# Kernel tuning notes

Hardware: AMD Instinct MI355X
Metric: run time of the kernel (lower is better)

Reference implementation:

```python
import jax, jax.numpy as jnp
import numpy as np

N = 20000   # nodes
E = 320000  # edges
T = 12      # sequence_length
H = 64      # hidden_dim
CIN = 16    # input_dim_per_step
L = 3       # num_st_layers
BN_EPS = 1e-5


def setup_inputs() -> dict:
    key = jax.random.key(0)
    ks = jax.random.split(key, 30)
    s = 0.05
    rn = lambda k, shp: jax.random.normal(k, shp, jnp.float32) * s
    inp = {
        "x": jax.random.normal(ks[0], (N, T * CIN), jnp.float32),
        "edge_index": jax.random.randint(ks[1], (2, E), 0, N, jnp.int32),
        # embedding
        "We": rn(ks[2], (CIN, H)), "be": rn(ks[3], (H,)),
        # stacked per-layer params for the 3 ST layers
        "gcn_W": rn(ks[4], (L, H, H)), "gcn_b": rn(ks[5], (L, H)),
        "conv_w": rn(ks[6], (L, H, H, 3)), "conv_b": rn(ks[7], (L, H)),
        "bn_g": jnp.ones((L, H), jnp.float32), "bn_b": rn(ks[8], (L, H)),
        "bn_m": rn(ks[9], (L, H)),
        "bn_v": jax.random.uniform(ks[10], (L, H), jnp.float32, 0.5, 1.5),
        # temporal attention MLP (H -> H//2 -> 1)
        "ta_w1": rn(ks[11], (H, H // 2)), "ta_b1": rn(ks[12], (H // 2,)),
        "ta_w2": rn(ks[13], (H // 2, 1)), "ta_b2": rn(ks[14], (1,)),
        # feature attention MLP (T -> T//2 -> 1)
        "fa_w1": rn(ks[15], (T, T // 2)), "fa_b1": rn(ks[16], (T // 2,)),
        "fa_w2": rn(ks[17], (T // 2, 1)), "fa_b2": rn(ks[18], (1,)),
        # output MLP (H -> H//2 -> 1)
        "ow1": rn(ks[19], (H, H // 2)), "ob1": rn(ks[20], (H // 2,)),
        "ow2": rn(ks[21], (H // 2, 1)), "ob2": rn(ks[22], (1,)),
    }
    return inp


def reference(x, edge_index, We, be, gcn_W, gcn_b, conv_w, conv_b,
              bn_g, bn_b, bn_m, bn_v, ta_w1, ta_b1, ta_w2, ta_b2,
              fa_w1, fa_b1, fa_w2, fa_b2, ow1, ob1, ow2, ob2):
    n = x.shape[0]
    # --- GCN normalization with self-loops (PyG gcn_norm) ---
    loops = jnp.arange(n, dtype=edge_index.dtype)
    src = jnp.concatenate([edge_index[0], loops])
    dst = jnp.concatenate([edge_index[1], loops])
    deg = jax.ops.segment_sum(jnp.ones_like(src, jnp.float32), dst, num_segments=n)
    dinv = 1.0 / jnp.sqrt(deg)  # deg >= 1 thanks to self-loops
    coef = dinv[src] * dinv[dst]  # [E+N]

    # --- per-timestep embedding (vectorized over t) ---
    xr = x.reshape(n, T, CIN)
    emb = jax.nn.relu(jnp.einsum('ntc,ch->nth', xr, We) + be)  # [N,T,H]
    x_st = emb.reshape(n, T * H)

    # --- ST layers (replicating original row-major .view layout mixing) ---
    for i in range(L):
        xi = x_st.reshape(n, H, T)  # [N,C,T]
        # GCNConv per timestep, batched over t: linear then normalized aggregate
        h = jnp.einsum('nct,cd->ndt', xi, gcn_W[i])          # [N,H,T]
        msg = coef[:, None, None] * h[src]                   # [E+N,H,T]
        agg = jax.ops.segment_sum(msg, dst, num_segments=n) + gcn_b[i][None, :, None]
        # temporal conv (kernel 3, pad 1) over T
        tmp = jax.lax.conv_general_dilated(
            agg, conv_w[i], (1,), [(1, 1)],
            dimension_numbers=('NCH', 'OIH', 'NCH')) + conv_b[i][None, :, None]
        # BatchNorm1d (eval mode: running stats)
        normed = (tmp - bn_m[i][None, :, None]) / jnp.sqrt(bn_v[i][None, :, None] + BN_EPS)
        normed = normed * bn_g[i][None, :, None] + bn_b[i][None, :, None]
        # residual is Identity (in_channels == out_channels)
        x_st = jax.nn.relu(normed + xi).reshape(n, H * T)

    # --- dual attention pooling ---
    xa = x_st.reshape(n, T, H)
    tw = (jnp.einsum('ntm,mk->ntk', jax.nn.relu(jnp.einsum('nth,hm->ntm', xa, ta_w1) + ta_b1), ta_w2) + ta_b2)[..., 0]
    tw = jax.nn.softmax(tw, axis=1)                          # [N,T]
    xt = (xa * tw[..., None]).transpose(0, 2, 1)             # [N,H,T]
    fw = (jnp.einsum('nhm,mk->nhk', jax.nn.relu(jnp.einsum('nht,tm->nhm', xt, fa_w1) + fa_b1), fa_w2) + fa_b2)[..., 0]
    fw = jax.nn.softmax(fw, axis=1)                          # [N,H]
    x_final = jnp.sum(xt * fw[..., None], axis=2)            # [N,H]

    # --- output MLP (dropout is identity in eval) ---
    out = jax.nn.relu(x_final @ ow1 + ob1) @ ow2 + ob2       # [N,1]
    return out
```

## Files before the change

kernel.cpp:

```cpp
#include <hip/hip_runtime.h>
#include <cstddef>
#include <cstdint>

#define T_ 12
#define H_ 64
#define CIN_ 16
#define F_ 768
#define BN_EPS 1e-5f
#define ECAP 80
#define RPITCH 88
#define SLOTS 64

typedef float v2f __attribute__((ext_vector_type(2)));
typedef short s8v __attribute__((ext_vector_type(8)));
typedef float f4v __attribute__((ext_vector_type(4)));

__device__ __forceinline__ unsigned short f2bf(float f) {
    unsigned u = __float_as_uint(f);
    unsigned r = (u + 0x7FFFu + ((u >> 16) & 1u)) >> 16;
    return (unsigned short)r;
}
__device__ __forceinline__ float bf2f(unsigned short h) {
    return __uint_as_float(((unsigned)h) << 16);
}
__device__ __forceinline__ v2f bf2x2(unsigned u) {
    v2f r;
    r.x = __uint_as_float(u << 16);
    r.y = __uint_as_float(u & 0xFFFF0000u);
    return r;
}
__device__ __forceinline__ v2f pkfma(v2f a, v2f b, v2f c) {
    return __builtin_elementwise_fma(a, b, c);
}


__global__ void k_init(int* __restrict__ cursor, int n) {
    int i = blockIdx.x * 256 + threadIdx.x;
    if (i < n) cursor[i] = 0;
}


__global__ __launch_bounds__(256) void k_fused(
        const float* __restrict__ gcn_W, const float* __restrict__ gcn_b,
        const float* __restrict__ conv_w,
        float* __restrict__ wkp, float* __restrict__ bkp,
        const int* __restrict__ srcv, const int* __restrict__ dstv,
        int* __restrict__ cursor, int* __restrict__ csr_src, int e,
        const float* __restrict__ x, const float* __restrict__ We,
        const float* __restrict__ be, unsigned short* __restrict__ xbf, int nT,
        int nbE) {
    __shared__ float sW[CIN_ * H_];
    __shared__ float sb[H_];
    int b = blockIdx.x;
    int tid = threadIdx.x;

    if (b < 36) {
        int l = b / 12, k = (b / 4) % 3, cq = b & 3;
        const float* Wg = gcn_W + (size_t)l * 4096;
        const float* cw = conv_w + (size_t)l * 12288;
#pragma unroll
        for (int j = 0; j < 4; j++) {
            int idx = j * 256 + tid;
            int c = cq * 16 + (idx >> 6);
            int o = idx & 63;
            float acc = 0.f;
            for (int d = 0; d < 64; d++)
                acc += Wg[c * 64 + d] * cw[(size_t)(o * 64 + d) * 3 + k];
            wkp[(((size_t)l * 3 + k) * 64 + c) * 64 + o] = acc;
        }
        if (cq == 0 && tid < 64) {
            int o = tid;
            const float* gb = gcn_b + (size_t)l * 64;
            float acc = 0.f;
            for (int d = 0; d < 64; d++)
                acc += gb[d] * cw[(size_t)(o * 64 + d) * 3 + k];
            bkp[((size_t)l * 3 + k) * 64 + o] = acc;
        }
        return;
    }
    if (b < 36 + nbE) {
        int i = (b - 36) * 256 + tid;
        if (i < e) {
            int d = dstv[i], s = srcv[i];
            int pos = atomicAdd(&cursor[d], 1);
            if (pos < SLOTS) csr_src[d * SLOTS + pos] = s;
        }
        return;
    }
    for (int i = tid; i < CIN_ * H_; i += 256) sW[i] = We[i];
    if (tid < H_) sb[tid] = be[tid];
    __syncthreads();
    int h4  = tid & 15;
    int ntl = tid >> 4;
    int nt  = (b - 36 - nbE) * 16 + ntl;
    if (nt >= nT) return;
    const float4* xp = (const float4*)(x + (size_t)nt * CIN_);
    float4 xv4[4];
    xv4[0] = xp[0]; xv4[1] = xp[1]; xv4[2] = xp[2]; xv4[3] = xp[3];
    const float* xs = (const float*)xv4;
    float acc[4];
#pragma unroll
    for (int j = 0; j < 4; j++) acc[j] = sb[h4 * 4 + j];
#pragma unroll
    for (int c = 0; c < CIN_; c++) {
        float4 w = *(const float4*)&sW[c * H_ + h4 * 4];
        float xc = xs[c];
        acc[0] += xc * w.x; acc[1] += xc * w.y;
        acc[2] += xc * w.z; acc[3] += xc * w.w;
    }
    ushort4 h;
    h.x = f2bf(fmaxf(acc[0], 0.f)); h.y = f2bf(fmaxf(acc[1], 0.f));
    h.z = f2bf(fmaxf(acc[2], 0.f)); h.w = f2bf(fmaxf(acc[3], 0.f));
    *(ushort4*)&xbf[(size_t)nt * H_ + h4 * 4] = h;
}


__global__ __launch_bounds__(256) void k_post(
        const float* __restrict__ wkp, unsigned short* __restrict__ wkA,
        const int* __restrict__ cursor, const int* __restrict__ csr_src,
        float* __restrict__ csr_coef, float* __restrict__ dinv, int n) {
    int b = blockIdx.x;
    int tid = threadIdx.x;
    if (b < 18) {
        int wave = tid >> 6, lane = tid & 63;
        int job = b * 4 + wave;
        int l = job / 24, rem = job % 24;
        int mt = rem / 6, ks = rem % 6;
        int o = mt * 16 + (lane & 15);
        int kbase = ks * 32 + (lane >> 4) * 8;
#pragma unroll
        for (int j = 0; j < 8; j++) {
            int k = kbase + j;
            int kk = k >> 6, c = k & 63;
            float v = wkp[(((size_t)l * 3 + kk) * 64 + c) * 64 + o];
            wkA[((((size_t)l * 24) + mt * 6 + ks) * 64 + lane) * 8 + j] = f2bf(v);
        }
        return;
    }
    int i = (b - 18) * 256 + tid;
    int node = i >> 6, slot = i & 63;
    if (node >= n) return;
    int deg = cursor[node];
    float dn = rsqrtf((float)(deg + 1));
    if (slot == 0) dinv[node] = dn;
    if (slot < min(deg, SLOTS)) {
        int s = csr_src[node * SLOTS + slot];
        csr_coef[node * SLOTS + slot] = rsqrtf((float)(cursor[s] + 1)) * dn;
    }
}


#define EDGE_LOAD(P, Q0, Q1) { \
    const unsigned short* rp_ = xin + (size_t)(P).x * F_; \
    Q0 = *(const uint4*)(rp_ + (lane << 3)); \
    Q1 = *(const uint2*)(rp_ + 512 + (lane << 2)); }

#define EDGE_FMA(P, Q0, Q1) { \
    float c_ = __int_as_float((P).y); \
    v2f c2_ = {c_, c_}; \
    a0 = pkfma(bf2x2((Q0).x), c2_, a0); a1 = pkfma(bf2x2((Q0).y), c2_, a1); \
    a2 = pkfma(bf2x2((Q0).z), c2_, a2); a3 = pkfma(bf2x2((Q0).w), c2_, a3); \
    a4 = pkfma(bf2x2((Q1).x), c2_, a4); a5 = pkfma(bf2x2((Q1).y), c2_, a5); }

#define LAYER_GATHER_CONV()                                                    \
    int tid = threadIdx.x;                                                     \
    int n0 = blockIdx.x * 8;                                                   \
    int wave = tid >> 6, lane = tid & 63;                                      \
    int wbase = wave * (ECAP * 2);                                             \
    for (int i = tid; i < 8 * 2 * RPITCH; i += 256) {                          \
        int s = i / (2 * RPITCH);                                              \
        int r = i - s * (2 * RPITCH);                                          \
        int row = (r < RPITCH) ? 0 : 13;                                       \
        int c = (r < RPITCH) ? r : r - RPITCH;                                 \
        sxb[s * 14 * RPITCH + row * RPITCH + c] = 0;                           \
    }                                                                          \
    int begs[2], cnts[2], stgs[2], epos[2];                                    \
    {                                                                          \
        int pos = 0;                                                           \
        for (int si = 0; si < 2; si++) {                                       \
            int nn = n0 + wave * 2 + si; if (nn >= n) nn = n - 1;              \
            int beg = nn * SLOTS;                                              \
            int cnt = min(degv[nn], SLOTS);                                    \
            int stg = min(cnt, ECAP - pos);                                    \
            for (int i = lane; i < stg; i += 64) {                             \
                se[wbase + (pos + i) * 2]     = csr_src[beg + i];              \
                se[wbase + (pos + i) * 2 + 1] = __float_as_int(csr_coef[beg + i]); \
            }                                                                  \
            begs[si] = beg; cnts[si] = cnt; stgs[si] = stg; epos[si] = pos;    \
            pos += stg;                                                        \
        }                                                                      \
    }                                                                          \
    {                                                                          \
        int wof[12];                                                           \
        _Pragma("unroll")                                                      \
        for (int u = 0; u < 12; u++) {                                         \
            int idx = (u < 8) ? ((lane << 3) + u) : (512 + (lane << 2) + u - 8); \
            int c = idx / 12, t = idx - 12 * c;                                \
            wof[u] = (t + 1) * RPITCH + c;                                     \
        }                                                                      \
        for (int si = 0; si < 2; si++) {                                       \
            int s = wave * 2 + si;                                             \
            int nn = n0 + s; if (nn >= n) nn = n - 1;                          \
            float dn = dinv[nn];                                               \
            float cs = dn * dn;                                                \
            v2f cs2 = {cs, cs};                                                \
            const unsigned short* xr = xin + (size_t)nn * F_;                  \
            uint4 z0 = *(const uint4*)(xr + (lane << 3));                      \
            uint2 z1 = *(const uint2*)(xr + 512 + (lane << 2));                \
            v2f a0 = bf2x2(z0.x) * cs2, a1 = bf2x2(z0.y) * cs2;                \
            v2f a2 = bf2x2(z0.z) * cs2, a3 = bf2x2(z0.w) * cs2;                \
            v2f a4 = bf2x2(z1.x) * cs2, a5 = bf2x2(z1.y) * cs2;                \
            int cnt = stgs[si];                                                \
            int base = wbase + epos[si] * 2;                                   \
            int e = 0;                                                         \
            for (; e + 3 < cnt; e += 4) {                                      \
                int2 pA = *(const int2*)&se[base + e * 2];                     \
                int2 pB = *(const int2*)&se[base + e * 2 + 2];                 \
                int2 pC = *(const int2*)&se[base + e * 2 + 4];                 \
                int2 pD = *(const int2*)&se[base + e * 2 + 6];                 \
                uint4 qA0; uint2 qA1; EDGE_LOAD(pA, qA0, qA1)                  \
                uint4 qB0; uint2 qB1; EDGE_LOAD(pB, qB0, qB1)                  \
                uint4 qC0; uint2 qC1; EDGE_LOAD(pC, qC0, qC1)                  \
                uint4 qD0; uint2 qD1; EDGE_LOAD(pD, qD0, qD1)                  \
                EDGE_FMA(pA, qA0, qA1)                                         \
                EDGE_FMA(pB, qB0, qB1)                                         \
                EDGE_FMA(pC, qC0, qC1)                                         \
                EDGE_FMA(pD, qD0, qD1)                                         \
            }                                                                  \
            for (; e < cnt; e++) {                                             \
                int2 pA = *(const int2*)&se[base + e * 2];                     \
                uint4 qA0; uint2 qA1; EDGE_LOAD(pA, qA0, qA1)                  \
                EDGE_FMA(pA, qA0, qA1)                                         \
            }                                                                  \
            for (int g = begs[si] + stgs[si]; g < begs[si] + cnts[si]; g++) {  \
                int2 pA; pA.x = csr_src[g];                                    \
                pA.y = __float_as_int(csr_coef[g]);                            \
                uint4 qA0; uint2 qA1; EDGE_LOAD(pA, qA0, qA1)                  \
                EDGE_FMA(pA, qA0, qA1)                                         \
            }                                                                  \
            unsigned short* wp0 = &sxb[s * 14 * RPITCH];                       \
            wp0[wof[0]]  = f2bf(a0.x); wp0[wof[1]]  = f2bf(a0.y);              \
            wp0[wof[2]]  = f2bf(a1.x); wp0[wof[3]]  = f2bf(a1.y);              \
            wp0[wof[4]]  = f2bf(a2.x); wp0[wof[5]]  = f2bf(a2.y);              \
            wp0[wof[6]]  = f2bf(a3.x); wp0[wof[7]]  = f2bf(a3.y);              \
            wp0[wof[8]]  = f2bf(a4.x); wp0[wof[9]]  = f2bf(a4.y);              \
            wp0[wof[10]] = f2bf(a5.x); wp0[wof[11]] = f2bf(a5.y);              \
        }                                                                      \
    }                                                                          \
    __syncthreads();                                                           \
    int mt = wave;                                                             \
    int q = lane >> 4;                                                         \
    int l15 = lane & 15;                                                       \
    s8v afr[6];                                                                \
    const s8v* Ap = (const s8v*)wkA;                                           \
    for (int ks = 0; ks < 6; ks++) afr[ks] = Ap[(mt * 6 + ks) * 64 + lane];    \
    int obase = mt * 16 + q * 4;                                               \
    float scl[4], shf[4], ball[4], bk0a[4], bk2a[4];                           \
    for (int r = 0; r < 4; r++) {                                              \
        int o = obase + r;                                                     \
        float sc = bng[o] * rsqrtf(bnv[o] + BN_EPS);                           \
        scl[r] = sc;                                                           \
        shf[r] = bnb[o] - bnm[o] * sc;                                         \
        float b0 = bkp[o], b1 = bkp[64 + o], b2 = bkp[128 + o];                \
        ball[r] = cb[o] + b0 + b1 + b2;                                        \
        bk0a[r] = b0; bk2a[r] = b2;                                            \
    }                                                                          \
    f4v accv[6];                                                               \
    for (int nt = 0; nt < 6; nt++) {                                           \
        int nidx = nt * 16 + l15;                                              \
        int s = nidx / 12, t = nidx - 12 * s;                                  \
        const s8v* bp = (const s8v*)&sxb[s * 14 * RPITCH + t * RPITCH + q * 8];\
        f4v acc = {0.f, 0.f, 0.f, 0.f};                                        \
        acc = __builtin_amdgcn_mfma_f32_16x16x32_bf16(afr[0], bp[0],  acc, 0, 0, 0); \
        acc = __builtin_amdgcn_mfma_f32_16x16x32_bf16(afr[1], bp[4],  acc, 0, 0, 0); \
        acc = __builtin_amdgcn_mfma_f32_16x16x32_bf16(afr[2], bp[11], acc, 0, 0, 0); \
        acc = __builtin_amdgcn_mfma_f32_16x16x32_bf16(afr[3], bp[15], acc, 0, 0, 0); \
        acc = __builtin_amdgcn_mfma_f32_16x16x32_bf16(afr[4], bp[22], acc, 0, 0, 0); \
        acc = __builtin_amdgcn_mfma_f32_16x16x32_bf16(afr[5], bp[26], acc, 0, 0, 0); \
        accv[nt] = acc;                                                        \
    }                                                                          \
    __syncthreads();                                                           \
    for (int nt = 0; nt < 6; nt++) {                                           \
        int nidx = nt * 16 + l15;                                              \
        int s = nidx / 12, t = nidx - 12 * s;                                  \
        unsigned short* dp = &sxb[s * F_ + t];                                 \
        for (int r = 0; r < 4; r++) {                                          \
            float bias = ball[r];                                              \
            if (t == 0)  bias -= bk0a[r];                                      \
            if (t == 11) bias -= bk2a[r];                                      \
            float v = (accv[nt][r] + bias) * scl[r] + shf[r];                  \
            dp[(obase + r) * 12] = f2bf(v);                                    \
        }                                                                      \
    }                                                                          \
    __syncthreads();


__global__ __launch_bounds__(256, 7) void k_layer(
        const unsigned short* __restrict__ xin,
        unsigned short* __restrict__ xout,
        const int* __restrict__ degv, const int* __restrict__ csr_src,
        const float* __restrict__ csr_coef, const float* __restrict__ dinv,
        const unsigned short* __restrict__ wkA,
        const float* __restrict__ bkp, const float* __restrict__ cb,
        const float* __restrict__ bng, const float* __restrict__ bnb,
        const float* __restrict__ bnm, const float* __restrict__ bnv,
        int n) {
    __shared__ __align__(16) unsigned short sxb[8 * 14 * RPITCH];
    __shared__ int se[4 * ECAP * 2];
    LAYER_GATHER_CONV()

#pragma unroll
    for (int cidx = 0; cidx < 3; cidx++) {
        int c = cidx * 256 + tid;
        int s = c / 96, off = c - s * 96;
        int nn = n0 + s;
        if (nn >= n) continue;
        uint4 dv = *(const uint4*)&sxb[s * F_ + off * 8];
        uint4 rv = ((const uint4*)(xin + (size_t)nn * F_))[off];
        uint4 ov;
        unsigned* dvp = (unsigned*)&dv;
        unsigned* rvp = (unsigned*)&rv;
        unsigned* ovp = (unsigned*)&ov;
#pragma unroll
        for (int w = 0; w < 4; w++) {
            v2f d2 = bf2x2(dvp[w]);
            v2f r2 = bf2x2(rvp[w]);
            float lo = fmaxf(d2.x + r2.x, 0.f);
            float hi = fmaxf(d2.y + r2.y, 0.f);
            ovp[w] = (unsigned)f2bf(lo) | ((unsigned)f2bf(hi) << 16);
        }
        *(uint4*)(xout + (size_t)nn * F_ + off * 8) = ov;
    }
}


__global__ __launch_bounds__(256, 6) void k_layer_attn(
        const unsigned short* __restrict__ xin,
        const int* __restrict__ degv, const int* __restrict__ csr_src,
        const float* __restrict__ csr_coef, const float* __restrict__ dinv,
        const unsigned short* __restrict__ wkA,
        const float* __restrict__ bkp, const float* __restrict__ cb,
        const float* __restrict__ bng, const float* __restrict__ bnb,
        const float* __restrict__ bnm, const float* __restrict__ bnv,
        const float* __restrict__ taw1, const float* __restrict__ tab1,
        const float* __restrict__ taw2, const float* __restrict__ tab2,
        const float* __restrict__ faw1, const float* __restrict__ fab1,
        const float* __restrict__ faw2, const float* __restrict__ fab2,
        const float* __restrict__ ow1, const float* __restrict__ ob1,
        const float* __restrict__ ow2, const float* __restrict__ ob2,
        float* __restrict__ out, int n) {
    __shared__ __align__(16) unsigned short sxb[8 * 14 * RPITCH];
    __shared__ int se[4 * ECAP * 2];
    LAYER_GATHER_CONV()

#pragma unroll
    for (int cidx = 0; cidx < 3; cidx++) {
        int c = cidx * 256 + tid;
        int s = c / 96, off = c - s * 96;
        int nn = n0 + s; if (nn >= n) nn = n - 1;
        uint4 dv = *(const uint4*)&sxb[s * F_ + off * 8];
        uint4 rv = ((const uint4*)(xin + (size_t)nn * F_))[off];
        unsigned* dvp = (unsigned*)&dv;
        unsigned* rvp = (unsigned*)&rv;
#pragma unroll
        for (int w = 0; w < 4; w++) {
            v2f d2 = bf2x2(dvp[w]);
            v2f r2 = bf2x2(rvp[w]);
            float lo = fmaxf(d2.x + r2.x, 0.f);
            float hi = fmaxf(d2.y + r2.y, 0.f);
            dvp[w] = (unsigned)f2bf(lo) | ((unsigned)f2bf(hi) << 16);
        }
        *(uint4*)&sxb[s * F_ + off * 8] = dv;
    }
    __syncthreads();

    float* s_tw = (float*)se;
    float* s_xf = (float*)se + 96;

    {
        int s2 = tid >> 5, m = tid & 31;
        float bm = tab1[m];
        v2f aa0 = {bm, bm}, aa1 = aa0, aa2 = aa0;
        v2f aa3 = aa0, aa4 = aa0, aa5 = aa0;
        const unsigned short* xr = &sxb[s2 * F_];
        float tb2 = tab2[0];
        for (int hh = 0; hh < 64; hh++) {
            const uint2* xp2 = (const uint2*)&xr[hh * 12];
            uint2 w0 = xp2[0], w1 = xp2[1], w2 = xp2[2];
            float wv = taw1[hh * 32 + m];
            v2f wv2 = {wv, wv};
            aa0 = pkfma(bf2x2(w0.x), wv2, aa0);
            aa1 = pkfma(bf2x2(w0.y), wv2, aa1);
            aa2 = pkfma(bf2x2(w1.x), wv2, aa2);
            aa3 = pkfma(bf2x2(w1.y), wv2, aa3);
            aa4 = pkfma(bf2x2(w2.x), wv2, aa4);
            aa5 = pkfma(bf2x2(w2.y), wv2, aa5);
        }
        float w2v = taw2[m];
        float av[12] = {aa0.x, aa0.y, aa1.x, aa1.y, aa2.x, aa2.y,
                        aa3.x, aa3.y, aa4.x, aa4.y, aa5.x, aa5.y};
#pragma unroll
        for (int t = 0; t < 12; t++) {
            float p = fmaxf(av[t], 0.f) * w2v;
            p += __shfl_xor(p, 1); p += __shfl_xor(p, 2);
            p += __shfl_xor(p, 4); p += __shfl_xor(p, 8);
            p += __shfl_xor(p, 16);
            if (m == 0) s_tw[s2 * 12 + t] = p + tb2;
        }
    }
    __syncthreads();

    {
        float fb2 = fab2[0];
        for (int qi = 0; qi < 2; qi++) {
            int ss = wave * 2 + qi;
            float tw[12];
#pragma unroll
            for (int t = 0; t < 12; t++) tw[t] = s_tw[ss * 12 + t];
            float mx = tw[0];
#pragma unroll
            for (int t = 1; t < 12; t++) mx = fmaxf(mx, tw[t]);
            float sum = 0.f;
#pragma unroll
            for (int t = 0; t < 12; t++) { tw[t] = __expf(tw[t] - mx); sum += tw[t]; }
            float inv = 1.f / sum;
            const uint2* xp2 = (const uint2*)&sxb[ss * F_ + lane * 12];
            uint2 w0 = xp2[0], w1 = xp2[1], w2 = xp2[2];
            v2f x0 = bf2x2(w0.x), x1 = bf2x2(w0.y), x2 = bf2x2(w1.x);
            v2f x3 = bf2x2(w1.y), x4 = bf2x2(w2.x), x5 = bf2x2(w2.y);
            float xv[12] = {x0.x, x0.y, x1.x, x1.y, x2.x, x2.y,
                            x3.x, x3.y, x4.x, x4.y, x5.x, x5.y};
            float xt[12];
#pragma unroll
            for (int t = 0; t < 12; t++) xt[t] = xv[t] * tw[t] * inv;
            float lf = fb2;
#pragma unroll
            for (int mm = 0; mm < 6; mm++) {
                float v = fab1[mm];
#pragma unroll
                for (int t = 0; t < 12; t++) v += xt[t] * faw1[t * 6 + mm];
                lf += fmaxf(v, 0.f) * faw2[mm];
            }
            float m2v = lf;
#pragma unroll
            for (int off = 32; off >= 1; off >>= 1)
                m2v = fmaxf(m2v, __shfl_xor(m2v, off));
            float ev = __expf(lf - m2v);
            float sev = ev;
#pragma unroll
            for (int off = 32; off >= 1; off >>= 1) sev += __shfl_xor(sev, off);
            float fwv = ev / sev;
            float xs = 0.f;
#pragma unroll
            for (int t = 0; t < 12; t++) xs += xt[t];
            s_xf[ss * 65 + lane] = fwv * xs;
        }
    }
    __syncthreads();

    {
        int s2 = tid >> 5, m = tid & 31;
        float v = ob1[m];
        const float* xfp = &s_xf[s2 * 65];
        for (int hh = 0; hh < 64; hh++) v += xfp[hh] * ow1[hh * 32 + m];
        float p = fmaxf(v, 0.f) * ow2[m];
        p += __shfl_xor(p, 1); p += __shfl_xor(p, 2);
        p += __shfl_xor(p, 4); p += __shfl_xor(p, 8);
        p += __shfl_xor(p, 16);
        if (m == 0 && n0 + s2 < n) out[n0 + s2] = p + ob2[0];
    }
}


extern "C" void kernel_launch(void* const* d_in, const int* in_sizes, int n_in,
                              void* d_out, int out_size, void* d_ws, size_t ws_size,
                              hipStream_t stream) {
    const float* x      = (const float*)d_in[0];
    const int*   ei     = (const int*)d_in[1];
    const float* We     = (const float*)d_in[2];
    const float* be     = (const float*)d_in[3];
    const float* gcn_W  = (const float*)d_in[4];
    const float* gcn_b  = (const float*)d_in[5];
    const float* conv_w = (const float*)d_in[6];
    const float* conv_b = (const float*)d_in[7];
    const float* bn_g   = (const float*)d_in[8];
    const float* bn_b   = (const float*)d_in[9];
    const float* bn_m   = (const float*)d_in[10];
    const float* bn_v   = (const float*)d_in[11];
    const float* ta_w1  = (const float*)d_in[12];
    const float* ta_b1  = (const float*)d_in[13];
    const float* ta_w2  = (const float*)d_in[14];
    const float* ta_b2  = (const float*)d_in[15];
    const float* fa_w1  = (const float*)d_in[16];
    const float* fa_b1  = (const float*)d_in[17];
    const float* fa_w2  = (const float*)d_in[18];
    const float* fa_b2  = (const float*)d_in[19];
    const float* ow1    = (const float*)d_in[20];
    const float* ob1    = (const float*)d_in[21];
    const float* ow2    = (const float*)d_in[22];
    const float* ob2    = (const float*)d_in[23];

    int n = in_sizes[0] / (T_ * CIN_);
    int e = in_sizes[1] / 2;
    const int* srcv = ei;
    const int* dstv = ei + e;

    char* p = (char*)d_ws;
    auto take = [&](size_t bytes) -> void* {
        void* r = (void*)p;
        p += (bytes + 255) & ~(size_t)255;
        return r;
    };
    int*   cursor    = (int*)take((size_t)n * 4);
    float* dinv      = (float*)take((size_t)n * 4);
    int*   csr_src   = (int*)take((size_t)n * SLOTS * 4);
    float* csr_coef  = (float*)take((size_t)n * SLOTS * 4);
    float* wkp       = (float*)take((size_t)3 * 3 * 64 * 64 * 4);
    float* bkp       = (float*)take((size_t)3 * 3 * 64 * 4);
    unsigned short* wkA = (unsigned short*)take((size_t)3 * 24 * 64 * 8 * 2);
    unsigned short* xabf = (unsigned short*)take((size_t)n * F_ * 2);
    unsigned short* xbbf = (unsigned short*)take((size_t)n * F_ * 2);

    int nb_n = (n + 255) / 256;
    int nb_e = (e + 255) / 256;
    int nb8  = (n + 7) / 8;
    int nT   = n * T_;
    int nbM  = (nT + 15) / 16;

    k_init<<<nb_n, 256, 0, stream>>>(cursor, n);
    k_fused<<<36 + nb_e + nbM, 256, 0, stream>>>(
        gcn_W, gcn_b, conv_w, wkp, bkp,
        srcv, dstv, cursor, csr_src, e,
        x, We, be, xabf, nT, nb_e);
    k_post<<<18 + (n * SLOTS + 255) / 256, 256, 0, stream>>>(
        wkp, wkA, cursor, csr_src, csr_coef, dinv, n);

    k_layer<<<nb8, 256, 0, stream>>>(xabf, xbbf, cursor, csr_src, csr_coef,
                                     dinv, wkA, bkp, conv_b,
                                     bn_g, bn_b, bn_m, bn_v, n);
    k_layer<<<nb8, 256, 0, stream>>>(xbbf, xabf, cursor, csr_src, csr_coef,
                                     dinv, wkA + (size_t)1 * 24 * 64 * 8,
                                     bkp + (size_t)1 * 3 * 64,
                                     conv_b + (size_t)1 * H_,
                                     bn_g + (size_t)1 * H_, bn_b + (size_t)1 * H_,
                                     bn_m + (size_t)1 * H_, bn_v + (size_t)1 * H_,
                                     n);
    k_layer_attn<<<nb8, 256, 0, stream>>>(xabf, cursor, csr_src, csr_coef,
                                          dinv, wkA + (size_t)2 * 24 * 64 * 8,
                                          bkp + (size_t)2 * 3 * 64,
                                          conv_b + (size_t)2 * H_,
                                          bn_g + (size_t)2 * H_, bn_b + (size_t)2 * H_,
                                          bn_m + (size_t)2 * H_, bn_v + (size_t)2 * H_,
                                          ta_w1, ta_b1, ta_w2, ta_b2,
                                          fa_w1, fa_b1, fa_w2, fa_b2,
                                          ow1, ob1, ow2, ob2, (float*)d_out, n);
}
```

Baseline: 423.0 us.

## Double-buffer edge gather loads and relax launch bounds for more registers

Turns the edge gather loop into a software pipeline: one batch of four neighbor rows is loaded while the previous batch is accumulated, which keeps more memory requests in flight per wave. Source indices are pre-multiplied by the row stride when staged into shared memory, removing a multiply from each gather. Launch bounds drop to 4 waves per SIMD so the compiler has room for the two sets of load registers. The cost is lower occupancy, which reduces latency hiding across waves in exchange for more overlap within each wave. Source index times 768 still fits in int for 20000 nodes.

```diff
diff --git a/kernel.cpp b/kernel.cpp
--- a/kernel.cpp
+++ b/kernel.cpp
@@ -150,17 +150,43 @@
 }
 
 
-#define EDGE_LOAD(P, Q0, Q1) { \
-    const unsigned short* rp_ = xin + (size_t)(P).x * F_; \
-    Q0 = *(const uint4*)(rp_ + (lane << 3)); \
-    Q1 = *(const uint2*)(rp_ + 512 + (lane << 2)); }
-
-#define EDGE_FMA(P, Q0, Q1) { \
+#define DECLB(S) \
+    int2 pA##S, pB##S, pC##S, pD##S; \
+    uint4 qA##S, qB##S, qC##S, qD##S; \
+    uint2 rA##S, rB##S, rC##S, rD##S;
+
+#define LOADB(S, EB) { \
+    pA##S = *(const int2*)&se[base + (EB) * 2]; \
+    pB##S = *(const int2*)&se[base + (EB) * 2 + 2]; \
+    pC##S = *(const int2*)&se[base + (EB) * 2 + 4]; \
+    pD##S = *(const int2*)&se[base + (EB) * 2 + 6]; \
+    { \
+        const unsigned short* rpA_ = xin + pA##S.x; \
+        const unsigned short* rpB_ = xin + pB##S.x; \
+        const unsigned short* rpC_ = xin + pC##S.x; \
+        const unsigned short* rpD_ = xin + pD##S.x; \
+        qA##S = *(const uint4*)(rpA_ + (lane << 3)); \
+        rA##S = *(const uint2*)(rpA_ + 512 + (lane << 2)); \
+        qB##S = *(const uint4*)(rpB_ + (lane << 3)); \
+        rB##S = *(const uint2*)(rpB_ + 512 + (lane << 2)); \
+        qC##S = *(const uint4*)(rpC_ + (lane << 3)); \
+        rC##S = *(const uint2*)(rpC_ + 512 + (lane << 2)); \
+        qD##S = *(const uint4*)(rpD_ + (lane << 3)); \
+        rD##S = *(const uint2*)(rpD_ + 512 + (lane << 2)); \
+    } }
+
+#define FMA1(P, Q, R) { \
     float c_ = __int_as_float((P).y); \
     v2f c2_ = {c_, c_}; \
-    a0 = pkfma(bf2x2((Q0).x), c2_, a0); a1 = pkfma(bf2x2((Q0).y), c2_, a1); \
-    a2 = pkfma(bf2x2((Q0).z), c2_, a2); a3 = pkfma(bf2x2((Q0).w), c2_, a3); \
-    a4 = pkfma(bf2x2((Q1).x), c2_, a4); a5 = pkfma(bf2x2((Q1).y), c2_, a5); }
+    a0 = pkfma(bf2x2((Q).x), c2_, a0); a1 = pkfma(bf2x2((Q).y), c2_, a1); \
+    a2 = pkfma(bf2x2((Q).z), c2_, a2); a3 = pkfma(bf2x2((Q).w), c2_, a3); \
+    a4 = pkfma(bf2x2((R).x), c2_, a4); a5 = pkfma(bf2x2((R).y), c2_, a5); }
+
+#define CONSB(S) \
+    FMA1(pA##S, qA##S, rA##S) \
+    FMA1(pB##S, qB##S, rB##S) \
+    FMA1(pC##S, qC##S, rC##S) \
+    FMA1(pD##S, qD##S, rD##S)
 
 #define LAYER_GATHER_CONV()                                                    \
     int tid = threadIdx.x;                                                     \
@@ -183,7 +209,7 @@
             int cnt = min(degv[nn], SLOTS);                                    \
             int stg = min(cnt, ECAP - pos);                                    \
             for (int i = lane; i < stg; i += 64) {                             \
-                se[wbase + (pos + i) * 2]     = csr_src[beg + i];              \
+                se[wbase + (pos + i) * 2]     = csr_src[beg + i] * F_;         \
                 se[wbase + (pos + i) * 2 + 1] = __float_as_int(csr_coef[beg + i]); \
             }                                                                  \
             begs[si] = beg; cnts[si] = cnt; stgs[si] = stg; epos[si] = pos;    \
@@ -212,31 +238,40 @@
             v2f a4 = bf2x2(z1.x) * cs2, a5 = bf2x2(z1.y) * cs2;                \
             int cnt = stgs[si];                                                \
             int base = wbase + epos[si] * 2;                                   \
-            int e = 0;                                                         \
-            for (; e + 3 < cnt; e += 4) {                                      \
-                int2 pA = *(const int2*)&se[base + e * 2];                     \
-                int2 pB = *(const int2*)&se[base + e * 2 + 2];                 \
-                int2 pC = *(const int2*)&se[base + e * 2 + 4];                 \
-                int2 pD = *(const int2*)&se[base + e * 2 + 6];                 \
-                uint4 qA0; uint2 qA1; EDGE_LOAD(pA, qA0, qA1)                  \
-                uint4 qB0; uint2 qB1; EDGE_LOAD(pB, qB0, qB1)                  \
-                uint4 qC0; uint2 qC1; EDGE_LOAD(pC, qC0, qC1)                  \
-                uint4 qD0; uint2 qD1; EDGE_LOAD(pD, qD0, qD1)                  \
-                EDGE_FMA(pA, qA0, qA1)                                         \
-                EDGE_FMA(pB, qB0, qB1)                                         \
-                EDGE_FMA(pC, qC0, qC1)                                         \
-                EDGE_FMA(pD, qD0, qD1)                                         \
+            int nb4 = cnt >> 2;                                                \
+            int e = nb4 << 2;                                                  \
+            if (nb4 > 0) {                                                     \
+                DECLB(0) DECLB(1)                                              \
+                LOADB(0, 0)                                                    \
+                int e4 = 1;                                                    \
+                for (; e4 + 1 < nb4; e4 += 2) {                                \
+                    LOADB(1, e4 * 4)                                           \
+                    CONSB(0)                                                   \
+                    LOADB(0, e4 * 4 + 4)                                       \
+                    CONSB(1)                                                   \
+                }                                                              \
+                if (e4 < nb4) {                                                \
+                    LOADB(1, e4 * 4)                                           \
+                    CONSB(0)                                                   \
+                    CONSB(1)                                                   \
+                } else {                                                       \
+                    CONSB(0)                                                   \
+                }                                                              \
             }                                                                  \
             for (; e < cnt; e++) {                                             \
-                int2 pA = *(const int2*)&se[base + e * 2];                     \
-                uint4 qA0; uint2 qA1; EDGE_LOAD(pA, qA0, qA1)                  \
-                EDGE_FMA(pA, qA0, qA1)                                         \
+                int2 pT = *(const int2*)&se[base + e * 2];                     \
+                const unsigned short* rpT_ = xin + pT.x;                       \
+                uint4 qT = *(const uint4*)(rpT_ + (lane << 3));                \
+                uint2 rT = *(const uint2*)(rpT_ + 512 + (lane << 2));          \
+                FMA1(pT, qT, rT)                                               \
             }                                                                  \
             for (int g = begs[si] + stgs[si]; g < begs[si] + cnts[si]; g++) {  \
-                int2 pA; pA.x = csr_src[g];                                    \
-                pA.y = __float_as_int(csr_coef[g]);                            \
-                uint4 qA0; uint2 qA1; EDGE_LOAD(pA, qA0, qA1)                  \
-                EDGE_FMA(pA, qA0, qA1)                                         \
+                int2 pT; pT.x = csr_src[g] * F_;                               \
+                pT.y = __float_as_int(csr_coef[g]);                            \
+                const unsigned short* rpT_ = xin + pT.x;                       \
+                uint4 qT = *(const uint4*)(rpT_ + (lane << 3));                \
+                uint2 rT = *(const uint2*)(rpT_ + 512 + (lane << 2));          \
+                FMA1(pT, qT, rT)                                               \
             }                                                                  \
             unsigned short* wp0 = &sxb[s * 14 * RPITCH];                       \
             wp0[wof[0]]  = f2bf(a0.x); wp0[wof[1]]  = f2bf(a0.y);              \
@@ -295,7 +330,7 @@
     __syncthreads();
 
 
-__global__ __launch_bounds__(256, 7) void k_layer(
+__global__ __launch_bounds__(256, 4) void k_layer(
         const unsigned short* __restrict__ xin,
         unsigned short* __restrict__ xout,
         const int* __restrict__ degv, const int* __restrict__ csr_src,
@@ -334,7 +369,7 @@
 }
 
 
-__global__ __launch_bounds__(256, 6) void k_layer_attn(
+__global__ __launch_bounds__(256, 4) void k_layer_attn(
         const unsigned short* __restrict__ xin,
         const int* __restrict__ degv, const int* __restrict__ csr_src,
         const float* __restrict__ csr_coef, const float* __restrict__ dinv,
```

Measured after the change: 428.6 us. No clear change (+1.3%).
